# Kernel optimization log

Hardware: AMD Instinct MI355X
Metric: run time of the kernel (lower is better)

Reference implementation:

```python
import jax, jax.numpy as jnp
import numpy as np

N_NODES = 100000
N_EDGES = 1600000
NEG_SLOPE = 0.2  # DGL GATConv default leaky_relu slope
BN_EPS = 1e-5


def setup_inputs() -> dict:
    key = jax.random.key(0)
    ks = jax.random.split(key, 10)
    feats = jax.random.normal(ks[0], (N_NODES, 128), dtype=jnp.float32)
    src = jax.random.randint(ks[1], (N_EDGES,), 0, N_NODES, dtype=jnp.int64)
    dst = jax.random.randint(ks[2], (N_EDGES,), 0, N_NODES, dtype=jnp.int64)
    fc_w = jax.random.normal(ks[3], (256, 128), dtype=jnp.float32) * 0.05   # H*D x in_feats
    attn_l = jax.random.normal(ks[4], (4, 64), dtype=jnp.float32) * 0.05
    attn_r = jax.random.normal(ks[5], (4, 64), dtype=jnp.float32) * 0.05
    res_w = jax.random.normal(ks[6], (256, 128), dtype=jnp.float32) * 0.05  # residual projection
    bias = jax.random.normal(ks[7], (4, 64), dtype=jnp.float32) * 0.05
    gamma = jnp.ones((64,), dtype=jnp.float32)
    beta = jnp.zeros((64,), dtype=jnp.float32)
    return {"feats": feats, "src": src, "dst": dst, "fc_w": fc_w,
            "attn_l": attn_l, "attn_r": attn_r, "res_w": res_w,
            "bias": bias, "gamma": gamma, "beta": beta}


def reference(feats, src, dst, fc_w, attn_l, attn_r, res_w, bias, gamma, beta):
    N = feats.shape[0]
    H, D = attn_l.shape
    # projected features [N, H, D] (feat_drop is identity in eval mode)
    h = (feats @ fc_w.T).reshape(N, H, D)
    # per-node attention logits [N, H]
    el = jnp.sum(h * attn_l[None], axis=-1)
    er = jnp.sum(h * attn_r[None], axis=-1)
    # edge logits, leaky relu
    e = el[src] + er[dst]                       # [E, H]
    e = jnp.where(e > 0, e, NEG_SLOPE * e)
    # numerically stable segment softmax over incoming edges of each dst node
    m = jax.ops.segment_max(e, dst, num_segments=N)       # [N, H]
    ex = jnp.exp(e - m[dst])                               # [E, H]
    s = jax.ops.segment_sum(ex, dst, num_segments=N)       # [N, H]
    alpha = ex / s[dst]                                    # [E, H]
    # weighted message aggregation: scatter-add alpha * h_src into dst
    msg = h[src] * alpha[:, :, None]                       # [E, H, D]
    rst = jax.ops.segment_sum(msg, dst, num_segments=N)    # [N, H, D]
    # residual projection + bias + activation (elu)
    res = (feats @ res_w.T).reshape(N, H, D)
    rst = jax.nn.elu(rst + res + bias[None])
    # mean over heads -> [N, D]
    out = rst.mean(axis=1)
    # BatchNorm1d (training stats: biased variance over the node/batch axis)
    mu = out.mean(axis=0)
    var = out.var(axis=0)
    return (out - mu) * jax.lax.rsqrt(var + BN_EPS) * gamma + beta
```

## Files before the change

### kernel.cpp

```cpp
#include <hip/hip_runtime.h>

#define N_NODES 100000
#define N_EDGES 1600000
#define NEG_SLOPE 0.2f
#define BN_EPS 1e-5f

typedef __attribute__((ext_vector_type(8))) short short8;
typedef __attribute__((ext_vector_type(4))) float floatx4;

static const size_t OFF_AB   = 0;
static const size_t OFF_BB   = 25624576;
static const size_t OFF_H    = 25755648;
static const size_t OFF_RES  = 76956672;
static const size_t OFF_EL   = 128156672;
static const size_t OFF_ER   = 129757184;
static const size_t OFF_DEG  = 131357184;
static const size_t OFF_RS   = 131757184;
static const size_t OFF_CUR  = 132157568;
static const size_t OFF_ESRC = 132557568;
static const size_t OFF_BS   = 142157568;
static const size_t OFF_BN   = 142158080;

__device__ __forceinline__ unsigned short f2bf(float x) {
  unsigned int u = __float_as_uint(x);
  unsigned int r = (u + 0x7fffu + ((u >> 16) & 1u)) >> 16;
  return (unsigned short)r;
}
__device__ __forceinline__ float bf2f(unsigned short u) {
  return __uint_as_float(((unsigned int)u) << 16);
}

__global__ __launch_bounds__(256) void k_pre(
    const float* __restrict__ feats, const float* __restrict__ fc_w,
    const float* __restrict__ res_w, const int* __restrict__ dst,
    unsigned short* __restrict__ Ab, unsigned short* __restrict__ Bb,
    int* __restrict__ deg, unsigned short* __restrict__ hbuf,
    float* __restrict__ el)
{
  const int b = blockIdx.x;
  if (b < 6256) {
    int c = b * 256 + threadIdx.x;
    int r = c >> 4, j = c & 15;
    unsigned short v[8];
    if (r < N_NODES) {
      const float* p = feats + (size_t)r * 128 + j * 8;
      float4 a = *(const float4*)p, bb = *(const float4*)(p + 4);
      v[0]=f2bf(a.x); v[1]=f2bf(a.y); v[2]=f2bf(a.z); v[3]=f2bf(a.w);
      v[4]=f2bf(bb.x); v[5]=f2bf(bb.y); v[6]=f2bf(bb.z); v[7]=f2bf(bb.w);
    } else {
      for (int i = 0; i < 8; i++) v[i] = 0;
    }
    size_t idx = (size_t)(r >> 7) * 2048 + ((r >> 4) & 7) * 256 + (j >> 2) * 64
               + (r & 15) + 16 * (j & 3);
    *(short8*)(Ab + idx * 8) = *(short8*)v;
  } else if (b < 12506) {
    int e = (b - 6256) * 256 + threadIdx.x;
    if (e < N_EDGES) atomicAdd(&deg[dst[e]], 1);
  } else if (b < 12538) {
    int c = (b - 12506) * 256 + threadIdx.x;
    int n = c >> 4, j = c & 15;
    const float* W = (n < 256) ? (fc_w + (size_t)n * 128) : (res_w + (size_t)(n - 256) * 128);
    const float* p = W + j * 8;
    float4 a = *(const float4*)p, bb = *(const float4*)(p + 4);
    unsigned short v[8];
    v[0]=f2bf(a.x); v[1]=f2bf(a.y); v[2]=f2bf(a.z); v[3]=f2bf(a.w);
    v[4]=f2bf(bb.x); v[5]=f2bf(bb.y); v[6]=f2bf(bb.z); v[7]=f2bf(bb.w);
    size_t idx = (size_t)(n >> 7) * 2048 + ((n >> 4) & 7) * 256 + (j >> 2) * 64
               + (n & 15) + 16 * (j & 3);
    *(short8*)(Bb + idx * 8) = *(short8*)v;
  } else {
    const int t = threadIdx.x;
    hbuf[(size_t)N_NODES * 256 + t] = 0;
    if (t < 4) el[N_NODES * 4 + t] = -1e30f;
  }
}

__global__ __launch_bounds__(256) void k_mm(
    const unsigned short* __restrict__ Ab, const unsigned short* __restrict__ Bb,
    const float* __restrict__ bias, const float* __restrict__ attn_l,
    const float* __restrict__ attn_r,
    unsigned short* __restrict__ hbuf, unsigned short* __restrict__ resbuf,
    float* __restrict__ el, float* __restrict__ er)
{
  __shared__ unsigned short sA[16384];
  const int tid = threadIdx.x;
  const int w = tid >> 6, L = tid & 63;
  const int blk = blockIdx.x, nb = blockIdx.y;

  {
    const unsigned short* ga = Ab + (size_t)blk * 16384;
    #pragma unroll
    for (int i = 0; i < 8; i++) {
      int off = (i * 256 + w * 64) * 8;
      __builtin_amdgcn_global_load_lds(
          (const __attribute__((address_space(1))) unsigned int*)(ga + off + L * 8),
          (__attribute__((address_space(3))) unsigned int*)(sA + off),
          16, 0, 0);
    }
  }
  const int mh = w & 1, nh = w >> 1;
  floatx4 acc[4][4] = {};
  __syncthreads();

  const unsigned short* gb = Bb + ((size_t)nb * 2048 + nh * 4 * 256) * 8 + L * 8;
  #pragma unroll
  for (int s = 0; s < 4; s++) {
    short8 a[4], b[4];
    #pragma unroll
    for (int t = 0; t < 4; t++)
      a[t] = *(const short8*)(sA + ((mh * 4 + t) * 256 + s * 64 + L) * 8);
    #pragma unroll
    for (int t = 0; t < 4; t++)
      b[t] = *(const short8*)(gb + ((size_t)t * 256 + s * 64) * 8);
    #pragma unroll
    for (int mt = 0; mt < 4; mt++)
      #pragma unroll
      for (int nt = 0; nt < 4; nt++)
        acc[mt][nt] = __builtin_amdgcn_mfma_f32_16x16x32_bf16(a[mt], b[nt], acc[mt][nt], 0, 0, 0);
  }

  const int q = L >> 4, cn = L & 15;
  const int r0 = blk * 128 + mh * 64;
  if (nb < 2) {
    const int head = nb * 2 + nh;
    const int col0 = nb * 128 + nh * 64;
    float al[4], ar[4];
    #pragma unroll
    for (int nt = 0; nt < 4; nt++) {
      al[nt] = attn_l[head * 64 + nt * 16 + cn];
      ar[nt] = attn_r[head * 64 + nt * 16 + cn];
    }
    #pragma unroll
    for (int mt = 0; mt < 4; mt++)
      #pragma unroll
      for (int r = 0; r < 4; r++) {
        const int row = r0 + mt * 16 + q * 4 + r;
        float pl = 0.f, pr = 0.f;
        #pragma unroll
        for (int nt = 0; nt < 4; nt++) {
          pl = fmaf(acc[mt][nt][r], al[nt], pl);
          pr = fmaf(acc[mt][nt][r], ar[nt], pr);
        }
        #pragma unroll
        for (int o = 1; o < 16; o <<= 1) {
          pl += __shfl_xor(pl, o, 64);
          pr += __shfl_xor(pr, o, 64);
        }
        if (row < N_NODES) {
          #pragma unroll
          for (int nt = 0; nt < 4; nt++)
            hbuf[(size_t)row * 256 + col0 + nt * 16 + cn] = f2bf(acc[mt][nt][r]);
          if (cn == 0) {
            el[row * 4 + head] = pl;
            er[row * 4 + head] = pr;
          }
        }
      }
  } else {
    const int rc0 = (nb - 2) * 128 + nh * 64;
    #pragma unroll
    for (int mt = 0; mt < 4; mt++)
      #pragma unroll
      for (int r = 0; r < 4; r++) {
        const int row = r0 + mt * 16 + q * 4 + r;
        if (row < N_NODES)
          #pragma unroll
          for (int nt = 0; nt < 4; nt++) {
            float v = acc[mt][nt][r] + bias[rc0 + nt * 16 + cn];
            resbuf[(size_t)row * 256 + rc0 + nt * 16 + cn] = f2bf(v);
          }
      }
  }
}

__global__ __launch_bounds__(256) void k_scan1(const int* __restrict__ deg,
                                               int* __restrict__ rs, int* __restrict__ bsums)
{
  __shared__ int tmp[256];
  const int t = threadIdx.x;
  const int base = blockIdx.x * 1024 + t * 4;
  int v0 = 0, v1 = 0, v2 = 0, v3 = 0;
  if (base + 0 < N_NODES) v0 = (deg[base + 0] + 3) & ~3;
  if (base + 1 < N_NODES) v1 = (deg[base + 1] + 3) & ~3;
  if (base + 2 < N_NODES) v2 = (deg[base + 2] + 3) & ~3;
  if (base + 3 < N_NODES) v3 = (deg[base + 3] + 3) & ~3;
  const int tsum = v0 + v1 + v2 + v3;
  tmp[t] = tsum;
  __syncthreads();
  for (int o = 1; o < 256; o <<= 1) {
    int x = (t >= o) ? tmp[t - o] : 0;
    __syncthreads();
    tmp[t] += x;
    __syncthreads();
  }
  const int excl = tmp[t] - tsum;
  if (base + 0 < N_NODES) rs[base + 0] = excl;
  if (base + 1 < N_NODES) rs[base + 1] = excl + v0;
  if (base + 2 < N_NODES) rs[base + 2] = excl + v0 + v1;
  if (base + 3 < N_NODES) rs[base + 3] = excl + v0 + v1 + v2;
  if (t == 255) bsums[blockIdx.x] = tmp[t];
}

__global__ __launch_bounds__(256) void k_scan3(int* __restrict__ rs,
                                               const int* __restrict__ bsums,
                                               int* __restrict__ cursor,
                                               const int* __restrict__ deg,
                                               int* __restrict__ esrc)
{
  __shared__ int sb[128];
  const int t = threadIdx.x;
  int raw = 0;
  if (t < 128) { raw = (t < 98) ? bsums[t] : 0; sb[t] = raw; }
  __syncthreads();
  for (int o = 1; o < 128; o <<= 1) {
    int x = (t >= o && t < 128) ? sb[t - o] : 0;
    __syncthreads();
    if (t < 128) sb[t] += x;
    __syncthreads();
  }
  if (t < 128) sb[t] -= raw;
  __syncthreads();
  const int i = blockIdx.x * 256 + t;
  if (i < N_NODES) {
    int v = rs[i] + sb[i >> 10];
    rs[i] = v;
    cursor[i] = v;
    const int d = deg[i];
    const int pd = (d + 3) & ~3;
    for (int j = d; j < pd; j++) esrc[v + j] = N_NODES;
    if (i == N_NODES - 1) rs[N_NODES] = v + pd;
  }
}

__global__ __launch_bounds__(256) void k_scatter(const int* __restrict__ src,
                                                 const int* __restrict__ dst,
                                                 int* __restrict__ cursor,
                                                 int* __restrict__ esrc)
{
  int e = blockIdx.x * 256 + threadIdx.x;
  if (e >= N_EDGES) return;
  int d = dst[e];
  int pos = atomicAdd(&cursor[d], 1);
  esrc[pos] = src[e];
}

#define RFL(x) __builtin_amdgcn_readfirstlane(x)

#define LOADSN4(SN, PP) do { SN = *(const int4*)(esrc + (PP)); } while (0)

#define GATHER4(EV, HV, SN) do { \
  const int g0_ = RFL(SN.x), g1_ = RFL(SN.y), g2_ = RFL(SN.z), g3_ = RFL(SN.w); \
  HV##0 = *(const ushort4*)(hbuf + (size_t)g0_ * 256 + lane4); \
  HV##1 = *(const ushort4*)(hbuf + (size_t)g1_ * 256 + lane4); \
  HV##2 = *(const ushort4*)(hbuf + (size_t)g2_ * 256 + lane4); \
  HV##3 = *(const ushort4*)(hbuf + (size_t)g3_ * 256 + lane4); \
  EV##0 = el[g0_ * 4 + head]; \
  EV##1 = el[g1_ * 4 + head]; \
  EV##2 = el[g2_ * 4 + head]; \
  EV##3 = el[g3_ * 4 + head]; \
} while (0)

#define EDGE1(EVi, HVi) do { \
  float e_ = EVi + ern; \
  e_ = (e_ > 0.f) ? e_ : NEG_SLOPE * e_; \
  const float w_ = __expf(e_); \
  ssum += w_; \
  acc.x = fmaf(w_, bf2f(HVi.x), acc.x); \
  acc.y = fmaf(w_, bf2f(HVi.y), acc.y); \
  acc.z = fmaf(w_, bf2f(HVi.z), acc.z); \
  acc.w = fmaf(w_, bf2f(HVi.w), acc.w); \
} while (0)

#define COMPUTE4(EV, HV) do { \
  EDGE1(EV##0, HV##0); EDGE1(EV##1, HV##1); \
  EDGE1(EV##2, HV##2); EDGE1(EV##3, HV##3); \
} while (0)

#define FIN(ND) do { \
  const float inv_ = (ssum > 0.f) ? (1.0f / ssum) : 0.f; \
  float vx_ = fmaf(acc.x, inv_, bf2f(rv_cur.x)); \
  float vy_ = fmaf(acc.y, inv_, bf2f(rv_cur.y)); \
  float vz_ = fmaf(acc.z, inv_, bf2f(rv_cur.z)); \
  float vw_ = fmaf(acc.w, inv_, bf2f(rv_cur.w)); \
  vx_ = (vx_ > 0.f) ? vx_ : (__expf(vx_) - 1.f); \
  vy_ = (vy_ > 0.f) ? vy_ : (__expf(vy_) - 1.f); \
  vz_ = (vz_ > 0.f) ? vz_ : (__expf(vz_) - 1.f); \
  vw_ = (vw_ > 0.f) ? vw_ : (__expf(vw_) - 1.f); \
  vx_ += __shfl_xor(vx_, 16, 64); vx_ += __shfl_xor(vx_, 32, 64); \
  vy_ += __shfl_xor(vy_, 16, 64); vy_ += __shfl_xor(vy_, 32, 64); \
  vz_ += __shfl_xor(vz_, 16, 64); vz_ += __shfl_xor(vz_, 32, 64); \
  vw_ += __shfl_xor(vw_, 16, 64); vw_ += __shfl_xor(vw_, 32, 64); \
  if (lane < 16) { \
    float4 o_; \
    o_.x = vx_ * 0.25f; o_.y = vy_ * 0.25f; o_.z = vz_ * 0.25f; o_.w = vw_ * 0.25f; \
    *(float4*)(out + (size_t)(ND) * 64 + lane4) = o_; \
  } \
} while (0)

#define BOUNDARY() \
  while (p == nend) { \
    FIN(nu); \
    acc.x = 0.f; acc.y = 0.f; acc.z = 0.f; acc.w = 0.f; ssum = 0.f; \
    nu++; \
    nend = nendN; ern = ernN; rv_cur = rvN; \
    const int f1_ = (nu + 1 < N_NODES) ? (nu + 1) : (N_NODES - 1); \
    const int f2_ = (nu + 2 <= N_NODES) ? (nu + 2) : N_NODES; \
    nendN = RFL(rs[f2_]); \
    ernN = er[f1_ * 4 + head]; \
    rvN = *(const ushort4*)(resbuf + (size_t)f1_ * 256 + lane4); \
  }

__global__ __launch_bounds__(256, 4) void k_agg(
    const unsigned short* __restrict__ hbuf, const unsigned short* __restrict__ resbuf,
    const float* __restrict__ el, const float* __restrict__ er,
    const int* __restrict__ rs, const int* __restrict__ esrc,
    float* __restrict__ out)
{
  const int lane = threadIdx.x & 63;
  const int head = lane >> 4;
  const int lane4 = lane * 4;
  const int wid = blockIdx.x * 4 + (threadIdx.x >> 6);
  const int nW = gridDim.x * 4;

  const int n0 = (int)(((long long)wid * N_NODES) / nW);
  const int n1 = (int)(((long long)(wid + 1) * N_NODES) / nW);
  if (n0 >= n1) return;

  int nu = RFL(n0);
  const int p_end = RFL(rs[n1]);
  int nend = RFL(rs[nu + 1]);
  {
  }
  int f1 = (nu + 1 < N_NODES) ? (nu + 1) : (N_NODES - 1);
  int f2 = (nu + 2 <= N_NODES) ? (nu + 2) : N_NODES;
  int nendN = RFL(rs[f2]);
  float ern  = er[nu * 4 + head];
  float ernN = er[f1 * 4 + head];
  ushort4 rv_cur = *(const ushort4*)(resbuf + (size_t)nu * 256 + lane4);
  ushort4 rvN    = *(const ushort4*)(resbuf + (size_t)f1 * 256 + lane4);

  float4 acc = make_float4(0.f, 0.f, 0.f, 0.f);
  float ssum = 0.f;

  int4 snA, snB, snC, snD;
  float evA0, evA1, evA2, evA3, evB0, evB1, evB2, evB3;
  float evC0, evC1, evC2, evC3, evD0, evD1, evD2, evD3;
  ushort4 hvA0, hvA1, hvA2, hvA3, hvB0, hvB1, hvB2, hvB3;
  ushort4 hvC0, hvC1, hvC2, hvC3, hvD0, hvD1, hvD2, hvD3;

  int p = RFL(rs[nu]);
  if (p      < p_end) { LOADSN4(snA, p);      GATHER4(evA, hvA, snA); }
  if (p + 4  < p_end) { LOADSN4(snB, p + 4);  GATHER4(evB, hvB, snB); }
  if (p + 8  < p_end) { LOADSN4(snC, p + 8);  GATHER4(evC, hvC, snC); }
  if (p + 12 < p_end) { LOADSN4(snD, p + 12); }

  while (p < p_end) {
    if (p + 12 < p_end) GATHER4(evD, hvD, snD);
    if (p + 16 < p_end) LOADSN4(snA, p + 16);
    BOUNDARY();
    COMPUTE4(evA, hvA);
    p += 4; if (p >= p_end) break;
    if (p + 12 < p_end) GATHER4(evA, hvA, snA);
    if (p + 16 < p_end) LOADSN4(snB, p + 16);
    BOUNDARY();
    COMPUTE4(evB, hvB);
    p += 4; if (p >= p_end) break;
    if (p + 12 < p_end) GATHER4(evB, hvB, snB);
    if (p + 16 < p_end) LOADSN4(snC, p + 16);
    BOUNDARY();
    COMPUTE4(evC, hvC);
    p += 4; if (p >= p_end) break;
    if (p + 12 < p_end) GATHER4(evC, hvC, snC);
    if (p + 16 < p_end) LOADSN4(snD, p + 16);
    BOUNDARY();
    COMPUTE4(evD, hvD);
    p += 4;
  }

  while (nu < n1) {
    FIN(nu);
    acc.x = 0.f; acc.y = 0.f; acc.z = 0.f; acc.w = 0.f; ssum = 0.f;
    nu++;
    if (nu < n1) rv_cur = *(const ushort4*)(resbuf + (size_t)nu * 256 + lane4);
  }
}

__global__ __launch_bounds__(256) void k_bn_stats(const float* __restrict__ out,
                                                  float* __restrict__ bn)
{
  const int t = threadIdx.x;
  const int c4 = (t & 15) * 4;
  const int rg = t >> 4;
  float4 s = make_float4(0.f, 0.f, 0.f, 0.f);
  float4 q = make_float4(0.f, 0.f, 0.f, 0.f);
  for (int row = blockIdx.x * 16 + rg; row < N_NODES; row += gridDim.x * 16) {
    float4 v = *(const float4*)(out + (size_t)row * 64 + c4);
    s.x += v.x; s.y += v.y; s.z += v.z; s.w += v.w;
    q.x += v.x * v.x; q.y += v.y * v.y; q.z += v.z * v.z; q.w += v.w * v.w;
  }
  __shared__ float ls[64], lq[64];
  if (t < 64) { ls[t] = 0.f; lq[t] = 0.f; }
  __syncthreads();
  atomicAdd(&ls[c4 + 0], s.x); atomicAdd(&ls[c4 + 1], s.y);
  atomicAdd(&ls[c4 + 2], s.z); atomicAdd(&ls[c4 + 3], s.w);
  atomicAdd(&lq[c4 + 0], q.x); atomicAdd(&lq[c4 + 1], q.y);
  atomicAdd(&lq[c4 + 2], q.z); atomicAdd(&lq[c4 + 3], q.w);
  __syncthreads();
  if (t < 64) {
    atomicAdd(&bn[t], ls[t]);
    atomicAdd(&bn[64 + t], lq[t]);
  }
}

__global__ __launch_bounds__(256) void k_bn_apply(float* __restrict__ out,
                                                  const float* __restrict__ bn,
                                                  const float* __restrict__ gamma,
                                                  const float* __restrict__ beta)
{
  __shared__ float sc[64], sh[64];
  const int t = threadIdx.x;
  if (t < 64) {
    float mean = bn[t] * (1.0f / N_NODES);
    float var = bn[64 + t] * (1.0f / N_NODES) - mean * mean;
    float s = gamma[t] * rsqrtf(var + BN_EPS);
    sc[t] = s;
    sh[t] = beta[t] - mean * s;
  }
  __syncthreads();
  const int i = blockIdx.x * 256 + t;
  if (i >= N_NODES * 16) return;
  const int d0 = (i & 15) * 4;
  float4 v = *(float4*)(out + (size_t)i * 4);
  v.x = fmaf(v.x, sc[d0 + 0], sh[d0 + 0]);
  v.y = fmaf(v.y, sc[d0 + 1], sh[d0 + 1]);
  v.z = fmaf(v.z, sc[d0 + 2], sh[d0 + 2]);
  v.w = fmaf(v.w, sc[d0 + 3], sh[d0 + 3]);
  *(float4*)(out + (size_t)i * 4) = v;
}

extern "C" void kernel_launch(void* const* d_in, const int* in_sizes, int n_in,
                              void* d_out, int out_size, void* d_ws, size_t ws_size,
                              hipStream_t stream)
{
  const float* feats  = (const float*)d_in[0];
  const int*   src    = (const int*)d_in[1];
  const int*   dst    = (const int*)d_in[2];
  const float* fc_w   = (const float*)d_in[3];
  const float* attn_l = (const float*)d_in[4];
  const float* attn_r = (const float*)d_in[5];
  const float* res_w  = (const float*)d_in[6];
  const float* bias   = (const float*)d_in[7];
  const float* gamma  = (const float*)d_in[8];
  const float* beta   = (const float*)d_in[9];

  char* ws = (char*)d_ws;
  unsigned short* Ab     = (unsigned short*)(ws + OFF_AB);
  unsigned short* Bb     = (unsigned short*)(ws + OFF_BB);
  unsigned short* hbuf   = (unsigned short*)(ws + OFF_H);
  unsigned short* resbuf = (unsigned short*)(ws + OFF_RES);
  float* elb    = (float*)(ws + OFF_EL);
  float* erb    = (float*)(ws + OFF_ER);
  int*   deg    = (int*)(ws + OFF_DEG);
  int*   rsb    = (int*)(ws + OFF_RS);
  int*   curb   = (int*)(ws + OFF_CUR);
  int*   esrc   = (int*)(ws + OFF_ESRC);
  int*   bsums  = (int*)(ws + OFF_BS);
  float* bnb    = (float*)(ws + OFF_BN);
  float* outp   = (float*)d_out;

  hipMemsetAsync(deg, 0, N_NODES * sizeof(int), stream);
  hipMemsetAsync(bnb, 0, 128 * sizeof(float), stream);

  k_pre<<<12539, 256, 0, stream>>>(feats, fc_w, res_w, dst, Ab, Bb, deg, hbuf, elb);
  k_mm<<<dim3(782, 4), 256, 0, stream>>>(Ab, Bb, bias, attn_l, attn_r,
                                         hbuf, resbuf, elb, erb);
  k_scan1<<<98, 256, 0, stream>>>(deg, rsb, bsums);
  k_scan3<<<391, 256, 0, stream>>>(rsb, bsums, curb, deg, esrc);
  k_scatter<<<6250, 256, 0, stream>>>(src, dst, curb, esrc);
  k_agg<<<2048, 256, 0, stream>>>(hbuf, resbuf, elb, erb, rsb, esrc, outp);
  k_bn_stats<<<256, 256, 0, stream>>>(outp, bnb);
  k_bn_apply<<<6250, 256, 0, stream>>>(outp, bnb, gamma, beta);
}
```

Measured before the change: 515.9 us.

## Record edge ranks during degree count, drop scatter atomics, halve matmul grid

The degree-count atomics now also record each edge's position within its destination segment into a scratch buffer aliased on the output. A new placement kernel then writes source indices directly, with no second round of atomics on a cursor array. The cursor buffer is removed. The matmul grid is halved so each block reuses its staged A tile for two column blocks. The aggregation kernel's occupancy hint rises from 4 to 8 blocks per SM, and the CSR build now runs before the matmul. Using the output buffer as rank scratch is safe only because aggregation overwrites it later. The higher occupancy hint may force register spills.

```diff
diff --git a/kernel.cpp b/kernel.cpp
--- a/kernel.cpp
+++ b/kernel.cpp
@@ -16,10 +16,9 @@
 static const size_t OFF_ER   = 129757184;
 static const size_t OFF_DEG  = 131357184;
 static const size_t OFF_RS   = 131757184;
-static const size_t OFF_CUR  = 132157568;
+static const size_t OFF_BN   = 132157568;
 static const size_t OFF_ESRC = 132557568;
 static const size_t OFF_BS   = 142157568;
-static const size_t OFF_BN   = 142158080;
 
 __device__ __forceinline__ unsigned short f2bf(float x) {
   unsigned int u = __float_as_uint(x);
@@ -35,7 +34,7 @@
     const float* __restrict__ res_w, const int* __restrict__ dst,
     unsigned short* __restrict__ Ab, unsigned short* __restrict__ Bb,
     int* __restrict__ deg, unsigned short* __restrict__ hbuf,
-    float* __restrict__ el)
+    float* __restrict__ el, int* __restrict__ rank)
 {
   const int b = blockIdx.x;
   if (b < 6256) {
@@ -55,7 +54,7 @@
     *(short8*)(Ab + idx * 8) = *(short8*)v;
   } else if (b < 12506) {
     int e = (b - 6256) * 256 + threadIdx.x;
-    if (e < N_EDGES) atomicAdd(&deg[dst[e]], 1);
+    if (e < N_EDGES) rank[e] = atomicAdd(&deg[dst[e]], 1);
   } else if (b < 12538) {
     int c = (b - 12506) * 256 + threadIdx.x;
     int n = c >> 4, j = c & 15;
@@ -75,6 +74,77 @@
   }
 }
 
+__global__ __launch_bounds__(256) void k_scan1(const int* __restrict__ deg,
+                                               int* __restrict__ rs, int* __restrict__ bsums)
+{
+  __shared__ int tmp[256];
+  const int t = threadIdx.x;
+  const int base = blockIdx.x * 1024 + t * 4;
+  int v0 = 0, v1 = 0, v2 = 0, v3 = 0;
+  if (base + 0 < N_NODES) v0 = (deg[base + 0] + 3) & ~3;
+  if (base + 1 < N_NODES) v1 = (deg[base + 1] + 3) & ~3;
+  if (base + 2 < N_NODES) v2 = (deg[base + 2] + 3) & ~3;
+  if (base + 3 < N_NODES) v3 = (deg[base + 3] + 3) & ~3;
+  const int tsum = v0 + v1 + v2 + v3;
+  tmp[t] = tsum;
+  __syncthreads();
+  for (int o = 1; o < 256; o <<= 1) {
+    int x = (t >= o) ? tmp[t - o] : 0;
+    __syncthreads();
+    tmp[t] += x;
+    __syncthreads();
+  }
+  const int excl = tmp[t] - tsum;
+  if (base + 0 < N_NODES) rs[base + 0] = excl;
+  if (base + 1 < N_NODES) rs[base + 1] = excl + v0;
+  if (base + 2 < N_NODES) rs[base + 2] = excl + v0 + v1;
+  if (base + 3 < N_NODES) rs[base + 3] = excl + v0 + v1 + v2;
+  if (t == 255) bsums[blockIdx.x] = tmp[t];
+}
+
+__global__ __launch_bounds__(256) void k_scan3(int* __restrict__ rs,
+                                               const int* __restrict__ bsums,
+                                               const int* __restrict__ deg,
+                                               int* __restrict__ esrc)
+{
+  __shared__ int sb[128];
+  const int t = threadIdx.x;
+  int raw = 0;
+  if (t < 128) { raw = (t < 98) ? bsums[t] : 0; sb[t] = raw; }
+  __syncthreads();
+  for (int o = 1; o < 128; o <<= 1) {
+    int x = (t >= o && t < 128) ? sb[t - o] : 0;
+    __syncthreads();
+    if (t < 128) sb[t] += x;
+    __syncthreads();
+  }
+  if (t < 128) sb[t] -= raw;
+  __syncthreads();
+  const int i = blockIdx.x * 256 + t;
+  if (i < N_NODES) {
+    int v = rs[i] + sb[i >> 10];
+    rs[i] = v;
+    const int d = deg[i];
+    const int pd = (d + 3) & ~3;
+    for (int j = d; j < pd; j++) esrc[v + j] = N_NODES;
+    if (i == N_NODES - 1) {
+      rs[N_NODES] = v + pd;
+      for (int j = 0; j < 16; j++) esrc[v + pd + j] = N_NODES;
+    }
+  }
+}
+
+__global__ __launch_bounds__(256) void k_place(const int* __restrict__ src,
+                                               const int* __restrict__ dst,
+                                               const int* __restrict__ rs,
+                                               const int* __restrict__ rank,
+                                               int* __restrict__ esrc)
+{
+  int e = blockIdx.x * 256 + threadIdx.x;
+  if (e >= N_EDGES) return;
+  esrc[rs[dst[e]] + rank[e]] = src[e];
+}
+
 __global__ __launch_bounds__(256) void k_mm(
     const unsigned short* __restrict__ Ab, const unsigned short* __restrict__ Bb,
     const float* __restrict__ bias, const float* __restrict__ attn_l,
@@ -85,7 +155,7 @@
   __shared__ unsigned short sA[16384];
   const int tid = threadIdx.x;
   const int w = tid >> 6, L = tid & 63;
-  const int blk = blockIdx.x, nb = blockIdx.y;
+  const int blk = blockIdx.x;
 
   {
     const unsigned short* ga = Ab + (size_t)blk * 16384;
@@ -99,149 +169,81 @@
     }
   }
   const int mh = w & 1, nh = w >> 1;
-  floatx4 acc[4][4] = {};
-  __syncthreads();
-
-  const unsigned short* gb = Bb + ((size_t)nb * 2048 + nh * 4 * 256) * 8 + L * 8;
-  #pragma unroll
-  for (int s = 0; s < 4; s++) {
-    short8 a[4], b[4];
+  __syncthreads();
+
+  for (int wb = 0; wb < 2; ++wb) {
+    const int nb = blockIdx.y + wb * 2;
+    floatx4 acc[4][4] = {};
+    const unsigned short* gb = Bb + ((size_t)nb * 2048 + nh * 4 * 256) * 8 + L * 8;
     #pragma unroll
-    for (int t = 0; t < 4; t++)
-      a[t] = *(const short8*)(sA + ((mh * 4 + t) * 256 + s * 64 + L) * 8);
-    #pragma unroll
-    for (int t = 0; t < 4; t++)
-      b[t] = *(const short8*)(gb + ((size_t)t * 256 + s * 64) * 8);
-    #pragma unroll
-    for (int mt = 0; mt < 4; mt++)
-      #pragma unroll
-      for (int nt = 0; nt < 4; nt++)
-        acc[mt][nt] = __builtin_amdgcn_mfma_f32_16x16x32_bf16(a[mt], b[nt], acc[mt][nt], 0, 0, 0);
-  }
-
-  const int q = L >> 4, cn = L & 15;
-  const int r0 = blk * 128 + mh * 64;
-  if (nb < 2) {
-    const int head = nb * 2 + nh;
-    const int col0 = nb * 128 + nh * 64;
-    float al[4], ar[4];
-    #pragma unroll
-    for (int nt = 0; nt < 4; nt++) {
-      al[nt] = attn_l[head * 64 + nt * 16 + cn];
-      ar[nt] = attn_r[head * 64 + nt * 16 + cn];
+    for (int s = 0; s < 4; s++) {
+      short8 a[4], b[4];
+      #pragma unroll
+      for (int t = 0; t < 4; t++)
+        a[t] = *(const short8*)(sA + ((mh * 4 + t) * 256 + s * 64 + L) * 8);
+      #pragma unroll
+      for (int t = 0; t < 4; t++)
+        b[t] = *(const short8*)(gb + ((size_t)t * 256 + s * 64) * 8);
+      #pragma unroll
+      for (int mt = 0; mt < 4; mt++)
+        #pragma unroll
+        for (int nt = 0; nt < 4; nt++)
+          acc[mt][nt] = __builtin_amdgcn_mfma_f32_16x16x32_bf16(a[mt], b[nt], acc[mt][nt], 0, 0, 0);
     }
-    #pragma unroll
-    for (int mt = 0; mt < 4; mt++)
-      #pragma unroll
-      for (int r = 0; r < 4; r++) {
-        const int row = r0 + mt * 16 + q * 4 + r;
-        float pl = 0.f, pr = 0.f;
+
+    const int q = L >> 4, cn = L & 15;
+    const int r0 = blk * 128 + mh * 64;
+    if (nb < 2) {
+      const int head = nb * 2 + nh;
+      const int col0 = nb * 128 + nh * 64;
+      float al[4], ar[4];
+      #pragma unroll
+      for (int nt = 0; nt < 4; nt++) {
+        al[nt] = attn_l[head * 64 + nt * 16 + cn];
+        ar[nt] = attn_r[head * 64 + nt * 16 + cn];
+      }
+      #pragma unroll
+      for (int mt = 0; mt < 4; mt++)
         #pragma unroll
-        for (int nt = 0; nt < 4; nt++) {
-          pl = fmaf(acc[mt][nt][r], al[nt], pl);
-          pr = fmaf(acc[mt][nt][r], ar[nt], pr);
-        }
-        #pragma unroll
-        for (int o = 1; o < 16; o <<= 1) {
-          pl += __shfl_xor(pl, o, 64);
-          pr += __shfl_xor(pr, o, 64);
-        }
-        if (row < N_NODES) {
+        for (int r = 0; r < 4; r++) {
+          const int row = r0 + mt * 16 + q * 4 + r;
+          float pl = 0.f, pr = 0.f;
           #pragma unroll
-          for (int nt = 0; nt < 4; nt++)
-            hbuf[(size_t)row * 256 + col0 + nt * 16 + cn] = f2bf(acc[mt][nt][r]);
-          if (cn == 0) {
-            el[row * 4 + head] = pl;
-            er[row * 4 + head] = pr;
+          for (int nt = 0; nt < 4; nt++) {
+            pl = fmaf(acc[mt][nt][r], al[nt], pl);
+            pr = fmaf(acc[mt][nt][r], ar[nt], pr);
+          }
+          #pragma unroll
+          for (int o = 1; o < 16; o <<= 1) {
+            pl += __shfl_xor(pl, o, 64);
+            pr += __shfl_xor(pr, o, 64);
+          }
+          if (row < N_NODES) {
+            #pragma unroll
+            for (int nt = 0; nt < 4; nt++)
+              hbuf[(size_t)row * 256 + col0 + nt * 16 + cn] = f2bf(acc[mt][nt][r]);
+            if (cn == 0) {
+              el[row * 4 + head] = pl;
+              er[row * 4 + head] = pr;
+            }
           }
         }
-      }
-  } else {
-    const int rc0 = (nb - 2) * 128 + nh * 64;
-    #pragma unroll
-    for (int mt = 0; mt < 4; mt++)
-      #pragma unroll
-      for (int r = 0; r < 4; r++) {
-        const int row = r0 + mt * 16 + q * 4 + r;
-        if (row < N_NODES)
-          #pragma unroll
-          for (int nt = 0; nt < 4; nt++) {
-            float v = acc[mt][nt][r] + bias[rc0 + nt * 16 + cn];
-            resbuf[(size_t)row * 256 + rc0 + nt * 16 + cn] = f2bf(v);
-          }
-      }
-  }
-}
-
-__global__ __launch_bounds__(256) void k_scan1(const int* __restrict__ deg,
-                                               int* __restrict__ rs, int* __restrict__ bsums)
-{
-  __shared__ int tmp[256];
-  const int t = threadIdx.x;
-  const int base = blockIdx.x * 1024 + t * 4;
-  int v0 = 0, v1 = 0, v2 = 0, v3 = 0;
-  if (base + 0 < N_NODES) v0 = (deg[base + 0] + 3) & ~3;
-  if (base + 1 < N_NODES) v1 = (deg[base + 1] + 3) & ~3;
-  if (base + 2 < N_NODES) v2 = (deg[base + 2] + 3) & ~3;
-  if (base + 3 < N_NODES) v3 = (deg[base + 3] + 3) & ~3;
-  const int tsum = v0 + v1 + v2 + v3;
-  tmp[t] = tsum;
-  __syncthreads();
-  for (int o = 1; o < 256; o <<= 1) {
-    int x = (t >= o) ? tmp[t - o] : 0;
-    __syncthreads();
-    tmp[t] += x;
-    __syncthreads();
-  }
-  const int excl = tmp[t] - tsum;
-  if (base + 0 < N_NODES) rs[base + 0] = excl;
-  if (base + 1 < N_NODES) rs[base + 1] = excl + v0;
-  if (base + 2 < N_NODES) rs[base + 2] = excl + v0 + v1;
-  if (base + 3 < N_NODES) rs[base + 3] = excl + v0 + v1 + v2;
-  if (t == 255) bsums[blockIdx.x] = tmp[t];
-}
-
-__global__ __launch_bounds__(256) void k_scan3(int* __restrict__ rs,
-                                               const int* __restrict__ bsums,
-                                               int* __restrict__ cursor,
-                                               const int* __restrict__ deg,
-                                               int* __restrict__ esrc)
-{
-  __shared__ int sb[128];
-  const int t = threadIdx.x;
-  int raw = 0;
-  if (t < 128) { raw = (t < 98) ? bsums[t] : 0; sb[t] = raw; }
-  __syncthreads();
-  for (int o = 1; o < 128; o <<= 1) {
-    int x = (t >= o && t < 128) ? sb[t - o] : 0;
-    __syncthreads();
-    if (t < 128) sb[t] += x;
-    __syncthreads();
-  }
-  if (t < 128) sb[t] -= raw;
-  __syncthreads();
-  const int i = blockIdx.x * 256 + t;
-  if (i < N_NODES) {
-    int v = rs[i] + sb[i >> 10];
-    rs[i] = v;
-    cursor[i] = v;
-    const int d = deg[i];
-    const int pd = (d + 3) & ~3;
-    for (int j = d; j < pd; j++) esrc[v + j] = N_NODES;
-    if (i == N_NODES - 1) rs[N_NODES] = v + pd;
-  }
-}
-
-__global__ __launch_bounds__(256) void k_scatter(const int* __restrict__ src,
-                                                 const int* __restrict__ dst,
-                                                 int* __restrict__ cursor,
-                                                 int* __restrict__ esrc)
-{
-  int e = blockIdx.x * 256 + threadIdx.x;
-  if (e >= N_EDGES) return;
-  int d = dst[e];
-  int pos = atomicAdd(&cursor[d], 1);
-  esrc[pos] = src[e];
+    } else {
+      const int rc0 = (nb - 2) * 128 + nh * 64;
+      #pragma unroll
+      for (int mt = 0; mt < 4; mt++)
+        #pragma unroll
+        for (int r = 0; r < 4; r++) {
+          const int row = r0 + mt * 16 + q * 4 + r;
+          if (row < N_NODES)
+            #pragma unroll
+            for (int nt = 0; nt < 4; nt++) {
+              float v = acc[mt][nt][r] + bias[rc0 + nt * 16 + cn];
+              resbuf[(size_t)row * 256 + rc0 + nt * 16 + cn] = f2bf(v);
+            }
+        }
+    }
+  }
 }
 
 #define RFL(x) __builtin_amdgcn_readfirstlane(x)
@@ -310,7 +312,7 @@
     rvN = *(const ushort4*)(resbuf + (size_t)f1_ * 256 + lane4); \
   }
 
-__global__ __launch_bounds__(256, 4) void k_agg(
+__global__ __launch_bounds__(256, 8) void k_agg(
     const unsigned short* __restrict__ hbuf, const unsigned short* __restrict__ resbuf,
     const float* __restrict__ el, const float* __restrict__ er,
     const int* __restrict__ rs, const int* __restrict__ esrc,
@@ -329,8 +331,6 @@
   int nu = RFL(n0);
   const int p_end = RFL(rs[n1]);
   int nend = RFL(rs[nu + 1]);
-  {
-  }
   int f1 = (nu + 1 < N_NODES) ? (nu + 1) : (N_NODES - 1);
   int f2 = (nu + 2 <= N_NODES) ? (nu + 2) : N_NODES;
   int nendN = RFL(rs[f2]);
@@ -462,21 +462,21 @@
   float* erb    = (float*)(ws + OFF_ER);
   int*   deg    = (int*)(ws + OFF_DEG);
   int*   rsb    = (int*)(ws + OFF_RS);
-  int*   curb   = (int*)(ws + OFF_CUR);
+  float* bnb    = (float*)(ws + OFF_BN);
   int*   esrc   = (int*)(ws + OFF_ESRC);
   int*   bsums  = (int*)(ws + OFF_BS);
-  float* bnb    = (float*)(ws + OFF_BN);
   float* outp   = (float*)d_out;
+  int*   rankp  = (int*)d_out;
 
   hipMemsetAsync(deg, 0, N_NODES * sizeof(int), stream);
   hipMemsetAsync(bnb, 0, 128 * sizeof(float), stream);
 
-  k_pre<<<12539, 256, 0, stream>>>(feats, fc_w, res_w, dst, Ab, Bb, deg, hbuf, elb);
-  k_mm<<<dim3(782, 4), 256, 0, stream>>>(Ab, Bb, bias, attn_l, attn_r,
+  k_pre<<<12539, 256, 0, stream>>>(feats, fc_w, res_w, dst, Ab, Bb, deg, hbuf, elb, rankp);
+  k_scan1<<<98, 256, 0, stream>>>(deg, rsb, bsums);
+  k_scan3<<<391, 256, 0, stream>>>(rsb, bsums, deg, esrc);
+  k_place<<<6250, 256, 0, stream>>>(src, dst, rsb, rankp, esrc);
+  k_mm<<<dim3(782, 2), 256, 0, stream>>>(Ab, Bb, bias, attn_l, attn_r,
                                          hbuf, resbuf, elb, erb);
-  k_scan1<<<98, 256, 0, stream>>>(deg, rsb, bsums);
-  k_scan3<<<391, 256, 0, stream>>>(rsb, bsums, curb, deg, esrc);
-  k_scatter<<<6250, 256, 0, stream>>>(src, dst, curb, esrc);
   k_agg<<<2048, 256, 0, stream>>>(hbuf, resbuf, elb, erb, rsb, esrc, outp);
   k_bn_stats<<<256, 256, 0, stream>>>(outp, bnb);
   k_bn_apply<<<6250, 256, 0, stream>>>(outp, bnb, gamma, beta);
```

After: 799.4 us. +55.0%, slower.
